# Performance work log

Hardware: AMD Instinct MI355X
Metric: run time of the kernel (lower is better)

Reference implementation:

```python
import jax, jax.numpy as jnp
import numpy as np

D_MODEL = 1024
N_HEADS = 16
HEAD_DIM = D_MODEL // N_HEADS


def setup_inputs() -> dict:
    key = jax.random.key(0)
    k1, k2, k3 = jax.random.split(key, 3)
    x = jax.random.normal(k1, (4, 2048, D_MODEL), dtype=jnp.float32)
    # torch Linear(d, 3d, bias=False): y = x @ W.T with W [3d, d]; store transposed [d, 3d]
    s = 1.0 / np.sqrt(D_MODEL)
    w_qkv = jax.random.uniform(k2, (D_MODEL, 3 * D_MODEL), dtype=jnp.float32, minval=-s, maxval=s)
    w_proj = jax.random.uniform(k3, (D_MODEL, D_MODEL), dtype=jnp.float32, minval=-s, maxval=s)
    return {"x": x, "w_qkv": w_qkv, "w_proj": w_proj}


def reference(x, w_qkv, w_proj):
    B, T, D = x.shape
    qkv = (x @ w_qkv).reshape(B, T, 3, N_HEADS, HEAD_DIM)
    qkv = jnp.transpose(qkv, (2, 0, 3, 1, 4))  # [3, B, H, T, hd]
    q, k, v = qkv[0], qkv[1], qkv[2]
    # NOTE: original module applies NO 1/sqrt(head_dim) scaling
    attn = jax.nn.softmax(jnp.einsum('bhqd,bhkd->bhqk', q, k), axis=-1)
    out = jnp.einsum('bhqk,bhkd->bhqd', attn, v)
    out = jnp.transpose(out, (0, 2, 1, 3)).reshape(B, T, D)
    return out @ w_proj
```

## Files before the change

kernel.cpp:

```cpp
#include <hip/hip_runtime.h>

typedef __bf16 bf16;
typedef __bf16 bf16x8 __attribute__((ext_vector_type(8)));
typedef float f32x4 __attribute__((ext_vector_type(4)));
typedef unsigned int uint;
typedef unsigned short ushort;

typedef const __attribute__((address_space(1))) void* gas_ptr;
typedef __attribute__((address_space(3))) void* las_ptr;

__device__ __forceinline__ void load16_lds(const void* g, void* l) {
  __builtin_amdgcn_global_load_lds((gas_ptr)g, (las_ptr)l, 16, 0, 0);
}

__global__ __launch_bounds__(256) void cast_f32_bf16(
    const float* __restrict__ in, bf16* __restrict__ out) {
  size_t i = (size_t)blockIdx.x * 256 + threadIdx.x;
  const float4* p = reinterpret_cast<const float4*>(in) + i * 2;
  float4 a = p[0], b = p[1];
  bf16x8 v;
  v[0] = (bf16)a.x; v[1] = (bf16)a.y; v[2] = (bf16)a.z; v[3] = (bf16)a.w;
  v[4] = (bf16)b.x; v[5] = (bf16)b.y; v[6] = (bf16)b.z; v[7] = (bf16)b.w;
  reinterpret_cast<bf16x8*>(out)[i] = v;
}

__global__ __launch_bounds__(256) void transpose_f32_bf16(
    const float* __restrict__ in, bf16* __restrict__ out, int K, int N) {
  __shared__ __attribute__((aligned(16))) bf16 tile[64 * 72];
  const int k0 = blockIdx.y * 64, n0 = blockIdx.x * 64;
  const int tid = threadIdx.x;
  for (int c = tid; c < 1024; c += 256) {
    int ki = c >> 4, j4 = c & 15;
    float4 f = *reinterpret_cast<const float4*>(in + (size_t)(k0 + ki) * N + n0 + j4 * 4);
    bf16* t = &tile[ki * 72 + j4 * 4];
    t[0] = (bf16)f.x; t[1] = (bf16)f.y; t[2] = (bf16)f.z; t[3] = (bf16)f.w;
  }
  __syncthreads();
  for (int c = tid; c < 512; c += 256) {
    int ni = c >> 3, k8 = c & 7;
    bf16x8 v;
    for (int j = 0; j < 8; j++) v[j] = tile[(k8 * 8 + j) * 72 + ni];
    *reinterpret_cast<bf16x8*>(out + (size_t)(n0 + ni) * K + k0 + k8 * 8) = v;
  }
}

template <typename CT>
__global__ __launch_bounds__(256, 2) void gemm_lds(
    const bf16* __restrict__ A, const bf16* __restrict__ Bt,
    CT* __restrict__ C, int M, int N, int K) {
  __shared__ __attribute__((aligned(16))) bf16 As[128 * 64];
  __shared__ __attribute__((aligned(16))) bf16 Bs[128 * 64];
  const int tid = threadIdx.x;
  const int wave = tid >> 6;
  const int lane = tid & 63;
  const int l15 = lane & 15;
  const int quad = lane >> 4;
  const int m0 = blockIdx.y * 128;
  const int n0 = blockIdx.x * 128;
  const int wm = (wave >> 1) * 64;
  const int wn = (wave & 1) * 64;

  f32x4 acc[4][4] = {};

  for (int kt = 0; kt < K; kt += 64) {
    __syncthreads();
    for (int it = 0; it < 4; ++it) {
      int p = it * 256 + wave * 64 + lane;
      int row = p >> 3, kc = (p & 7) ^ (row & 7);
      load16_lds(A + (size_t)(m0 + row) * K + kt + kc * 8, &As[p * 8]);
      load16_lds(Bt + (size_t)(n0 + row) * K + kt + kc * 8, &Bs[p * 8]);
    }
    __syncthreads();
    for (int kk = 0; kk < 64; kk += 32) {
      const int kc = (kk >> 3) + quad;
      bf16x8 af[4], bfr[4];
      for (int i = 0; i < 4; i++) {
        int row = wm + i * 16 + l15;
        af[i] = *reinterpret_cast<const bf16x8*>(&As[(row * 8 + (kc ^ (row & 7))) * 8]);
      }
      for (int j = 0; j < 4; j++) {
        int row = wn + j * 16 + l15;
        bfr[j] = *reinterpret_cast<const bf16x8*>(&Bs[(row * 8 + (kc ^ (row & 7))) * 8]);
      }
      for (int i = 0; i < 4; i++)
        for (int j = 0; j < 4; j++)
          acc[i][j] = __builtin_amdgcn_mfma_f32_16x16x32_bf16(af[i], bfr[j], acc[i][j], 0, 0, 0);
    }
  }

  for (int i = 0; i < 4; i++)
    for (int j = 0; j < 4; j++)
      for (int r = 0; r < 4; r++) {
        int row = m0 + wm + i * 16 + quad * 4 + r;
        int col = n0 + wn + j * 16 + l15;
        C[(size_t)row * N + col] = (CT)acc[i][j][r];
      }
}

__device__ __forceinline__ int vs_dw(int d, int kdw) {
  return d * 32 + (kdw ^ ((((d >> 3) ^ d) & 7) * 4));
}

__global__ __launch_bounds__(256, 4) void attn_kernel(
    const bf16* __restrict__ qkv, bf16* __restrict__ out) {
  __shared__ __attribute__((aligned(16))) bf16 Ks[64 * 64];
  __shared__ __attribute__((aligned(16))) uint Vs[64 * 32];

  const int tid = threadIdx.x;
  const int wave = tid >> 6;
  const int lane = tid & 63;
  const int l15 = lane & 15;
  const int quad = lane >> 4;
  const int b = blockIdx.x >> 4;
  const int h = blockIdx.x & 15;
  const int qt0 = blockIdx.y * 64;
  const bf16* base = qkv + (size_t)b * 2048 * 3072 + h * 64;
  const float L2E = 1.44269504f;

  bf16x8 aq0, aq1;
  {
    const bf16* qrow = base + (size_t)(qt0 + wave * 16 + l15) * 3072;
    aq0 = *reinterpret_cast<const bf16x8*>(qrow + quad * 8);
    aq1 = *reinterpret_cast<const bf16x8*>(qrow + 32 + quad * 8);
    for (int j = 0; j < 8; j++) {
      aq0[j] = (bf16)((float)aq0[j] * L2E);
      aq1[j] = (bf16)((float)aq1[j] * L2E);
    }
  }

  bf16x8 bones = {};
  if (l15 == 0)
    for (int j = 0; j < 8; j++) bones[j] = (bf16)1.0f;

  float m_q = -1e30f;
  f32x4 o[4] = {};
  f32x4 l_acc = {};

  const int kp = tid >> 3;
  const int oct = tid & 7;
  const int kkey = tid >> 3;
  const int kk8 = tid & 7;
  const int prow = ((kkey & 4) << 2) | ((kkey & 24) >> 1) | (kkey & 3);
  const int kxor = kk8 ^ (prow & 7);
  const int kdst0 = (prow * 8 + kxor) * 8;
  const int kdst1 = kdst0 + 32 * 64;

  bf16x8 kpre0, kpre1, vpre0, vpre1;
  {
    const bf16* kb = base + 1024 + (size_t)kkey * 3072 + kk8 * 8;
    kpre0 = *reinterpret_cast<const bf16x8*>(kb);
    kpre1 = *reinterpret_cast<const bf16x8*>(kb + (size_t)32 * 3072);
    const bf16* v0p = base + (size_t)(2 * kp) * 3072 + 2048 + oct * 8;
    vpre0 = *reinterpret_cast<const bf16x8*>(v0p);
    vpre1 = *reinterpret_cast<const bf16x8*>(v0p + 3072);
  }

  for (int kt = 0; kt < 2048; kt += 64) {
    __syncthreads();
    *reinterpret_cast<bf16x8*>(&Ks[kdst0]) = kpre0;
    *reinterpret_cast<bf16x8*>(&Ks[kdst1]) = kpre1;
    {
      const ushort* u0 = reinterpret_cast<const ushort*>(&vpre0);
      const ushort* u1 = reinterpret_cast<const ushort*>(&vpre1);
      for (int i = 0; i < 8; i++)
        Vs[vs_dw(oct * 8 + i, kp)] = (uint)u0[i] | ((uint)u1[i] << 16);
    }
    __syncthreads();

    if (kt + 64 < 2048) {
      const bf16* nb = base + (size_t)(kt + 64) * 3072;
      const bf16* kb = nb + 1024 + (size_t)kkey * 3072 + kk8 * 8;
      kpre0 = *reinterpret_cast<const bf16x8*>(kb);
      kpre1 = *reinterpret_cast<const bf16x8*>(kb + (size_t)32 * 3072);
      const bf16* v0p = nb + (size_t)(2 * kp) * 3072 + 2048 + oct * 8;
      vpre0 = *reinterpret_cast<const bf16x8*>(v0p);
      vpre1 = *reinterpret_cast<const bf16x8*>(v0p + 3072);
    }

    f32x4 s[4];
    __builtin_amdgcn_s_setprio(1);
    for (int n = 0; n < 4; n++) {
      int row = n * 16 + l15;
      int xr = row & 7;
      bf16x8 ak0 = *reinterpret_cast<const bf16x8*>(&Ks[(row * 8 + (quad ^ xr)) * 8]);
      bf16x8 ak1 = *reinterpret_cast<const bf16x8*>(&Ks[(row * 8 + ((4 + quad) ^ xr)) * 8]);
      f32x4 z = {};
      z = __builtin_amdgcn_mfma_f32_16x16x32_bf16(ak0, aq0, z, 0, 0, 0);
      z = __builtin_amdgcn_mfma_f32_16x16x32_bf16(ak1, aq1, z, 0, 0, 0);
      s[n] = z;
    }
    __builtin_amdgcn_s_setprio(0);

    float mt = fmaxf(fmaxf(s[0][0], s[0][1]), fmaxf(s[0][2], s[0][3]));
    mt = fmaxf(mt, fmaxf(fmaxf(s[1][0], s[1][1]), fmaxf(s[1][2], s[1][3])));
    mt = fmaxf(mt, fmaxf(fmaxf(s[2][0], s[2][1]), fmaxf(s[2][2], s[2][3])));
    mt = fmaxf(mt, fmaxf(fmaxf(s[3][0], s[3][1]), fmaxf(s[3][2], s[3][3])));
    mt = fmaxf(mt, __shfl_xor(mt, 16, 64));
    mt = fmaxf(mt, __shfl_xor(mt, 32, 64));

    if (!__all(mt - m_q <= 8.0f)) {
      float mn = fmaxf(m_q, mt);
      float alpha = __builtin_amdgcn_exp2f(m_q - mn);
      m_q = mn;
      float a0 = __shfl(alpha, quad * 4 + 0, 64);
      float a1 = __shfl(alpha, quad * 4 + 1, 64);
      float a2 = __shfl(alpha, quad * 4 + 2, 64);
      float a3 = __shfl(alpha, quad * 4 + 3, 64);
      l_acc[0] *= a0; l_acc[1] *= a1; l_acc[2] *= a2; l_acc[3] *= a3;
      for (int n = 0; n < 4; n++) {
        o[n][0] *= a0; o[n][1] *= a1; o[n][2] *= a2; o[n][3] *= a3;
      }
    }

    bf16x8 ap0, ap1;
    for (int r = 0; r < 4; r++) {
      ap0[r]     = (bf16)__builtin_amdgcn_exp2f(s[0][r] - m_q);
      ap0[4 + r] = (bf16)__builtin_amdgcn_exp2f(s[1][r] - m_q);
      ap1[r]     = (bf16)__builtin_amdgcn_exp2f(s[2][r] - m_q);
      ap1[4 + r] = (bf16)__builtin_amdgcn_exp2f(s[3][r] - m_q);
    }

    __builtin_amdgcn_s_setprio(1);
    l_acc = __builtin_amdgcn_mfma_f32_16x16x32_bf16(ap0, bones, l_acc, 0, 0, 0);
    l_acc = __builtin_amdgcn_mfma_f32_16x16x32_bf16(ap1, bones, l_acc, 0, 0, 0);

    for (int n = 0; n < 4; n++) {
      int d = n * 16 + l15;
      uint4 u0 = *reinterpret_cast<const uint4*>(&Vs[vs_dw(d, quad * 4)]);
      uint4 u1 = *reinterpret_cast<const uint4*>(&Vs[vs_dw(d, 16 + quad * 4)]);
      bf16x8 bv0 = *reinterpret_cast<const bf16x8*>(&u0);
      bf16x8 bv1 = *reinterpret_cast<const bf16x8*>(&u1);
      o[n] = __builtin_amdgcn_mfma_f32_16x16x32_bf16(ap0, bv0, o[n], 0, 0, 0);
      o[n] = __builtin_amdgcn_mfma_f32_16x16x32_bf16(ap1, bv1, o[n], 0, 0, 0);
    }
    __builtin_amdgcn_s_setprio(0);
  }

  for (int r = 0; r < 4; r++) {
    float lv = __shfl(l_acc[r], quad * 16, 64);
    float inv = 1.0f / lv;
    int q = qt0 + wave * 16 + quad * 4 + r;
    bf16* orow = out + (size_t)(b * 2048 + q) * 1024 + h * 64;
    for (int n = 0; n < 4; n++) orow[n * 16 + l15] = (bf16)(o[n][r] * inv);
  }
}

extern "C" void kernel_launch(void* const* d_in, const int* in_sizes, int n_in,
                              void* d_out, int out_size, void* d_ws, size_t ws_size,
                              hipStream_t stream) {
  const float* x = (const float*)d_in[0];
  const float* w_qkv = (const float*)d_in[1];
  const float* w_proj = (const float*)d_in[2];
  float* out = (float*)d_out;

  bf16* ws = (bf16*)d_ws;
  bf16* x_bf = ws;
  bf16* wqkvT = x_bf + (size_t)8192 * 1024;
  bf16* wprojT = wqkvT + 3072 * 1024;
  bf16* qkv = wprojT + 1024 * 1024;
  bf16* attn_out = qkv + (size_t)8192 * 3072;

  cast_f32_bf16<<<4096, 256, 0, stream>>>(x, x_bf);
  transpose_f32_bf16<<<dim3(48, 16), 256, 0, stream>>>(w_qkv, wqkvT, 1024, 3072);
  transpose_f32_bf16<<<dim3(16, 16), 256, 0, stream>>>(w_proj, wprojT, 1024, 1024);
  gemm_lds<bf16><<<dim3(24, 64), 256, 0, stream>>>(x_bf, wqkvT, qkv, 8192, 3072, 1024);
  attn_kernel<<<dim3(64, 32), 256, 0, stream>>>(qkv, attn_out);
  gemm_lds<float><<<dim3(8, 64), 256, 0, stream>>>(attn_out, wprojT, out, 8192, 1024, 1024);
}
```

Measured before the change: 281.8 us.

## Double-buffer attention K/V in LDS, widen blocks to 8 waves, swizzle GEMM tiles

The attention kernel now uses 512-thread blocks covering 128 query rows. K and V tiles are double-buffered in LDS, so each iteration needs one barrier instead of two, and half the waves stage V while the other half stage K. The GEMM remaps workgroup IDs in an 8-way interleave to improve L2 reuse between neighbouring tiles. The max reduction is also rewritten as a linear chain. The bigger blocks and doubled LDS use may lower occupancy.

```diff
diff --git a/kernel.cpp b/kernel.cpp
--- a/kernel.cpp
+++ b/kernel.cpp
@@ -55,8 +55,11 @@
   const int lane = tid & 63;
   const int l15 = lane & 15;
   const int quad = lane >> 4;
-  const int m0 = blockIdx.y * 128;
-  const int n0 = blockIdx.x * 128;
+  const int nwg = gridDim.x * gridDim.y;
+  const int orig = blockIdx.y * gridDim.x + blockIdx.x;
+  const int swz = (orig & 7) * (nwg >> 3) + (orig >> 3);
+  const int m0 = (swz / gridDim.x) * 128;
+  const int n0 = (swz % gridDim.x) * 128;
   const int wm = (wave >> 1) * 64;
   const int wn = (wave & 1) * 64;
 
@@ -101,10 +104,10 @@
   return d * 32 + (kdw ^ ((((d >> 3) ^ d) & 7) * 4));
 }
 
-__global__ __launch_bounds__(256, 4) void attn_kernel(
+__global__ __launch_bounds__(512, 4) void attn_kernel(
     const bf16* __restrict__ qkv, bf16* __restrict__ out) {
-  __shared__ __attribute__((aligned(16))) bf16 Ks[64 * 64];
-  __shared__ __attribute__((aligned(16))) uint Vs[64 * 32];
+  __shared__ __attribute__((aligned(16))) bf16 Ks[2][64 * 64];
+  __shared__ __attribute__((aligned(16))) uint Vs[2][64 * 32];
 
   const int tid = threadIdx.x;
   const int wave = tid >> 6;
@@ -113,7 +116,7 @@
   const int quad = lane >> 4;
   const int b = blockIdx.x >> 4;
   const int h = blockIdx.x & 15;
-  const int qt0 = blockIdx.y * 64;
+  const int qt0 = blockIdx.y * 128;
   const bf16* base = qkv + (size_t)b * 2048 * 3072 + h * 64;
   const float L2E = 1.44269504f;
 
@@ -136,45 +139,50 @@
   f32x4 o[4] = {};
   f32x4 l_acc = {};
 
-  const int kp = tid >> 3;
-  const int oct = tid & 7;
-  const int kkey = tid >> 3;
-  const int kk8 = tid & 7;
-  const int prow = ((kkey & 4) << 2) | ((kkey & 24) >> 1) | (kkey & 3);
-  const int kxor = kk8 ^ (prow & 7);
+  const int t2 = tid & 255;
+  const int kp = t2 >> 3;
+  const int oct = t2 & 7;
+  const bool vrole = (wave < 4);
+  const int prow = ((kp & 4) << 2) | ((kp & 24) >> 1) | (kp & 3);
+  const int kxor = oct ^ (prow & 7);
   const int kdst0 = (prow * 8 + kxor) * 8;
   const int kdst1 = kdst0 + 32 * 64;
 
-  bf16x8 kpre0, kpre1, vpre0, vpre1;
-  {
-    const bf16* kb = base + 1024 + (size_t)kkey * 3072 + kk8 * 8;
-    kpre0 = *reinterpret_cast<const bf16x8*>(kb);
-    kpre1 = *reinterpret_cast<const bf16x8*>(kb + (size_t)32 * 3072);
+  bf16x8 pre0, pre1;
+  if (vrole) {
     const bf16* v0p = base + (size_t)(2 * kp) * 3072 + 2048 + oct * 8;
-    vpre0 = *reinterpret_cast<const bf16x8*>(v0p);
-    vpre1 = *reinterpret_cast<const bf16x8*>(v0p + 3072);
+    pre0 = *reinterpret_cast<const bf16x8*>(v0p);
+    pre1 = *reinterpret_cast<const bf16x8*>(v0p + 3072);
+  } else {
+    const bf16* kb = base + 1024 + (size_t)kp * 3072 + oct * 8;
+    pre0 = *reinterpret_cast<const bf16x8*>(kb);
+    pre1 = *reinterpret_cast<const bf16x8*>(kb + (size_t)32 * 3072);
   }
 
   for (int kt = 0; kt < 2048; kt += 64) {
-    __syncthreads();
-    *reinterpret_cast<bf16x8*>(&Ks[kdst0]) = kpre0;
-    *reinterpret_cast<bf16x8*>(&Ks[kdst1]) = kpre1;
-    {
-      const ushort* u0 = reinterpret_cast<const ushort*>(&vpre0);
-      const ushort* u1 = reinterpret_cast<const ushort*>(&vpre1);
+    const int cur = (kt >> 6) & 1;
+    if (vrole) {
+      const ushort* u0 = reinterpret_cast<const ushort*>(&pre0);
+      const ushort* u1 = reinterpret_cast<const ushort*>(&pre1);
       for (int i = 0; i < 8; i++)
-        Vs[vs_dw(oct * 8 + i, kp)] = (uint)u0[i] | ((uint)u1[i] << 16);
+        Vs[cur][vs_dw(oct * 8 + i, kp)] = (uint)u0[i] | ((uint)u1[i] << 16);
+    } else {
+      *reinterpret_cast<bf16x8*>(&Ks[cur][kdst0]) = pre0;
+      *reinterpret_cast<bf16x8*>(&Ks[cur][kdst1]) = pre1;
     }
     __syncthreads();
 
     if (kt + 64 < 2048) {
       const bf16* nb = base + (size_t)(kt + 64) * 3072;
-      const bf16* kb = nb + 1024 + (size_t)kkey * 3072 + kk8 * 8;
-      kpre0 = *reinterpret_cast<const bf16x8*>(kb);
-      kpre1 = *reinterpret_cast<const bf16x8*>(kb + (size_t)32 * 3072);
-      const bf16* v0p = nb + (size_t)(2 * kp) * 3072 + 2048 + oct * 8;
-      vpre0 = *reinterpret_cast<const bf16x8*>(v0p);
-      vpre1 = *reinterpret_cast<const bf16x8*>(v0p + 3072);
+      if (vrole) {
+        const bf16* v0p = nb + (size_t)(2 * kp) * 3072 + 2048 + oct * 8;
+        pre0 = *reinterpret_cast<const bf16x8*>(v0p);
+        pre1 = *reinterpret_cast<const bf16x8*>(v0p + 3072);
+      } else {
+        const bf16* kb = nb + 1024 + (size_t)kp * 3072 + oct * 8;
+        pre0 = *reinterpret_cast<const bf16x8*>(kb);
+        pre1 = *reinterpret_cast<const bf16x8*>(kb + (size_t)32 * 3072);
+      }
     }
 
     f32x4 s[4];
@@ -182,8 +190,8 @@
     for (int n = 0; n < 4; n++) {
       int row = n * 16 + l15;
       int xr = row & 7;
-      bf16x8 ak0 = *reinterpret_cast<const bf16x8*>(&Ks[(row * 8 + (quad ^ xr)) * 8]);
-      bf16x8 ak1 = *reinterpret_cast<const bf16x8*>(&Ks[(row * 8 + ((4 + quad) ^ xr)) * 8]);
+      bf16x8 ak0 = *reinterpret_cast<const bf16x8*>(&Ks[cur][(row * 8 + (quad ^ xr)) * 8]);
+      bf16x8 ak1 = *reinterpret_cast<const bf16x8*>(&Ks[cur][(row * 8 + ((4 + quad) ^ xr)) * 8]);
       f32x4 z = {};
       z = __builtin_amdgcn_mfma_f32_16x16x32_bf16(ak0, aq0, z, 0, 0, 0);
       z = __builtin_amdgcn_mfma_f32_16x16x32_bf16(ak1, aq1, z, 0, 0, 0);
@@ -191,10 +199,14 @@
     }
     __builtin_amdgcn_s_setprio(0);
 
-    float mt = fmaxf(fmaxf(s[0][0], s[0][1]), fmaxf(s[0][2], s[0][3]));
-    mt = fmaxf(mt, fmaxf(fmaxf(s[1][0], s[1][1]), fmaxf(s[1][2], s[1][3])));
-    mt = fmaxf(mt, fmaxf(fmaxf(s[2][0], s[2][1]), fmaxf(s[2][2], s[2][3])));
-    mt = fmaxf(mt, fmaxf(fmaxf(s[3][0], s[3][1]), fmaxf(s[3][2], s[3][3])));
+    float mt = fmaxf(fmaxf(s[0][0], s[0][1]), s[0][2]);
+    mt = fmaxf(fmaxf(mt, s[0][3]), s[1][0]);
+    mt = fmaxf(fmaxf(mt, s[1][1]), s[1][2]);
+    mt = fmaxf(fmaxf(mt, s[1][3]), s[2][0]);
+    mt = fmaxf(fmaxf(mt, s[2][1]), s[2][2]);
+    mt = fmaxf(fmaxf(mt, s[2][3]), s[3][0]);
+    mt = fmaxf(fmaxf(mt, s[3][1]), s[3][2]);
+    mt = fmaxf(mt, s[3][3]);
     mt = fmaxf(mt, __shfl_xor(mt, 16, 64));
     mt = fmaxf(mt, __shfl_xor(mt, 32, 64));
 
@@ -226,8 +238,8 @@
 
     for (int n = 0; n < 4; n++) {
       int d = n * 16 + l15;
-      uint4 u0 = *reinterpret_cast<const uint4*>(&Vs[vs_dw(d, quad * 4)]);
-      uint4 u1 = *reinterpret_cast<const uint4*>(&Vs[vs_dw(d, 16 + quad * 4)]);
+      uint4 u0 = *reinterpret_cast<const uint4*>(&Vs[cur][vs_dw(d, quad * 4)]);
+      uint4 u1 = *reinterpret_cast<const uint4*>(&Vs[cur][vs_dw(d, 16 + quad * 4)]);
       bf16x8 bv0 = *reinterpret_cast<const bf16x8*>(&u0);
       bf16x8 bv1 = *reinterpret_cast<const bf16x8*>(&u1);
       o[n] = __builtin_amdgcn_mfma_f32_16x16x32_bf16(ap0, bv0, o[n], 0, 0, 0);
@@ -264,6 +276,6 @@
   transpose_f32_bf16<<<dim3(48, 16), 256, 0, stream>>>(w_qkv, wqkvT, 1024, 3072);
   transpose_f32_bf16<<<dim3(16, 16), 256, 0, stream>>>(w_proj, wprojT, 1024, 1024);
   gemm_lds<bf16><<<dim3(24, 64), 256, 0, stream>>>(x_bf, wqkvT, qkv, 8192, 3072, 1024);
-  attn_kernel<<<dim3(64, 32), 256, 0, stream>>>(qkv, attn_out);
+  attn_kernel<<<dim3(64, 16), 512, 0, stream>>>(qkv, attn_out);
   gemm_lds<float><<<dim3(8, 64), 256, 0, stream>>>(attn_out, wprojT, out, 8192, 1024, 1024);
 }
```

After: 276.4 us. About the same (-1.9%).
